# Optimization experiments

Hardware: AMD Instinct MI355X
Metric: run time of the kernel (lower is better)

The kernel has to match this reference:

```python
import jax, jax.numpy as jnp
import numpy as np

N_NODES = 256
DIM = 128
N_LAYERS = 3
LN_EPS = 1e-5


def setup_inputs() -> dict:
    key = jax.random.key(0)
    ks = jax.random.split(key, 8)
    B = 2048
    node_features = jax.random.normal(ks[0], (B, N_NODES, DIM), dtype=jnp.float32)
    A_logits_pos = jax.random.normal(ks[1], (N_NODES, N_NODES), dtype=jnp.float32) * 0.01
    A_logits_neg = jax.random.normal(ks[2], (N_NODES, N_NODES), dtype=jnp.float32) * 0.01
    # per-layer Linear weights, torch layout (out_dim, in_dim); all dims are 128
    scale = 1.0 / np.sqrt(DIM)
    W_pos = jax.random.uniform(ks[3], (N_LAYERS, DIM, DIM), jnp.float32, -scale, scale)
    W_neg = jax.random.uniform(ks[4], (N_LAYERS, DIM, DIM), jnp.float32, -scale, scale)
    ln_g = jnp.ones((N_LAYERS, DIM), jnp.float32)
    ln_b = jnp.zeros((N_LAYERS, DIM), jnp.float32)
    ro_g = jnp.ones((DIM,), jnp.float32)
    ro_b = jnp.zeros((DIM,), jnp.float32)
    return {"node_features": node_features, "A_logits_pos": A_logits_pos,
            "A_logits_neg": A_logits_neg, "W_pos": W_pos, "W_neg": W_neg,
            "ln_g": ln_g, "ln_b": ln_b, "ro_g": ro_g, "ro_b": ro_b}


def _layernorm(x, g, b):
    mu = jnp.mean(x, axis=-1, keepdims=True)
    var = jnp.var(x, axis=-1, keepdims=True)
    return (x - mu) * jax.lax.rsqrt(var + LN_EPS) * g + b


def reference(node_features, A_logits_pos, A_logits_neg, W_pos, W_neg, ln_g, ln_b, ro_g, ro_b):
    # soft signed adjacency with hard-mask split (mask is non-differentiable)
    A_p = jax.nn.sigmoid(A_logits_pos)
    A_n = jax.nn.sigmoid(A_logits_neg)
    mask = (A_p > A_n).astype(A_p.dtype)
    A_pos = A_p * mask
    A_neg = A_n * (1.0 - mask)

    H = node_features  # (B, N, D)
    for l in range(N_LAYERS):
        agg_pos = jnp.einsum('uv,bvd->bud', A_pos, H)
        agg_neg = jnp.einsum('uv,bvd->bud', A_neg, H)
        # torch Linear: x @ W.T ; GELU is exact (erf) by default in torch
        out = jax.nn.gelu(jnp.einsum('bud,od->buo', agg_pos, W_pos[l])
                          - jnp.einsum('bud,od->buo', agg_neg, W_neg[l]),
                          approximate=False)
        H = _layernorm(out, ln_g[l], ln_b[l])  # dropout = identity in eval

    h_G = jnp.mean(H, axis=1)  # (B, D) readout
    return _layernorm(h_G, ro_g, ro_b)
```

## Files before the change

kernel.cpp:

```cpp
#include <hip/hip_runtime.h>
#include <math.h>


typedef float  f32x4  __attribute__((ext_vector_type(4)));
typedef float  f32x16 __attribute__((ext_vector_type(16)));
typedef short  s16x8  __attribute__((ext_vector_type(8)));
typedef __bf16 bf16x8 __attribute__((ext_vector_type(8)));

#define GOFF 65536

__device__ __forceinline__ unsigned short f2bf(float f) {
  __bf16 h = (__bf16)f;
  return __builtin_bit_cast(unsigned short, h);
}
__device__ __forceinline__ float bf2f(unsigned short h) {
  return __builtin_bit_cast(float, (unsigned int)h << 16);
}
__device__ __forceinline__ unsigned short f2bf_rne(float f) {
  unsigned int u = __builtin_bit_cast(unsigned int, f);
  u = (u + 0x7fffu + ((u >> 16) & 1u)) >> 16;
  return (unsigned short)u;
}

__device__ __forceinline__ int haddr(int v, int d) {
  return v * 256 + ((d * 2) ^ ((v & 15) << 4));
}
__device__ __forceinline__ int gaddr(int o, int vr) {
  return GOFF + o * 80 + vr * 2;
}

#define MFMA32(a, b, c) __builtin_amdgcn_mfma_f32_32x32x16_bf16( \
    __builtin_bit_cast(bf16x8, (a)), __builtin_bit_cast(bf16x8, (b)), (c), 0, 0, 0)

__global__ void prep_kernel(const float* __restrict__ alp, const float* __restrict__ aln,
                            const float* __restrict__ wp,  const float* __restrict__ wn,
                            unsigned short* __restrict__ A3, unsigned short* __restrict__ W3) {
  int idx = blockIdx.x * 512 + threadIdx.x;
  if (idx < 131072) {
    int j = idx & 7, lane = (idx >> 3) & 63, vt = (idx >> 9) & 15,
        ut = (idx >> 13) & 7, h = (idx >> 16) & 1;
    int u = ut * 32 + (lane & 31);
    int v = vt * 16 + (lane >> 5) * 8 + j;
    int s = u * 256 + v;
    float ap = 1.f / (1.f + expf(-alp[s]));
    float an = 1.f / (1.f + expf(-aln[s]));
    bool  m  = ap > an;
    float val = h ? (m ? 0.f : -an) : (m ? ap : 0.f);
    A3[idx] = f2bf_rne(val);
  } else {
    int k = idx - 131072;
    int j = k & 7, lane = (k >> 3) & 63, kt = (k >> 9) & 7,
        ot = (k >> 12) & 3, hw = (k >> 14);
    int o = ot * 32 + (lane & 31);
    int d = kt * 16 + (lane >> 5) * 8 + j;
    const float* src = (hw & 1) ? wn : wp;
    W3[k] = f2bf_rne(src[(hw >> 1) * 16384 + o * 128 + d]);
  }
}

__global__ __launch_bounds__(256, 2) void gnn_kernel(
    const float* __restrict__ X,
    const unsigned short* __restrict__ A3,
    const unsigned short* __restrict__ W3,
    const float* __restrict__ ln_g, const float* __restrict__ ln_b,
    const float* __restrict__ ro_g, const float* __restrict__ ro_b,
    float* __restrict__ out) {
  extern __shared__ char smem[];
  const int tid  = threadIdx.x;
  const int wid  = tid >> 6;
  const int lane = tid & 63;
  const int l31  = lane & 31;
  const int hi   = lane >> 5;
  const int b    = blockIdx.x;

  {
    const float4* Xb = (const float4*)(X + (size_t)b * 256 * 128);
#pragma unroll 8
    for (int i = 0; i < 32; ++i) {
      int idx = tid + i * 256;
      int v = idx >> 5, d = (idx & 31) * 4;
      float4 f = Xb[idx];
      ushort4 p;
      p.x = f2bf(f.x); p.y = f2bf(f.y); p.z = f2bf(f.z); p.w = f2bf(f.w);
      *(ushort4*)(smem + haddr(v, d)) = p;
    }
  }
  __syncthreads();

  f32x16 acc[2][4];
  for (int l = 0; l < 3; ++l) {
#pragma unroll
    for (int mt = 0; mt < 2; ++mt)
#pragma unroll
      for (int nt = 0; nt < 4; ++nt)
#pragma unroll
        for (int r = 0; r < 16; ++r) acc[mt][nt][r] = 0.f;

    for (int h = 0; h < 2; ++h) {
      const unsigned short* Wb = W3 + (size_t)(((l * 2 + h) * 4 + wid) * 8) * 512;
      const unsigned short* Ab = A3 + (size_t)((h * 8 + wid * 2) * 16) * 512;

      for (int c = 0; c < 8; ++c) {
        s16x8 pa[4];
#pragma unroll
        for (int kt = 0; kt < 2; ++kt) {
          pa[kt * 2 + 0] = *(const s16x8*)(Ab + (size_t)(0 * 16 + c * 2 + kt) * 512 + lane * 8);
          pa[kt * 2 + 1] = *(const s16x8*)(Ab + (size_t)(1 * 16 + c * 2 + kt) * 512 + lane * 8);
        }

        f32x16 g0;
#pragma unroll
        for (int r = 0; r < 16; ++r) g0[r] = 0.f;
        const int v0 = c * 32 + l31;
#pragma unroll
        for (int kt = 0; kt < 8; ++kt) {
          s16x8 ha = *(const s16x8*)(smem + haddr(v0, kt * 16 + hi * 8));
          s16x8 wb = *(const s16x8*)(Wb + (size_t)kt * 512 + lane * 8);
          g0 = MFMA32(ha, wb, g0);
        }
        __syncthreads();
        {
          const int og = wid * 32 + l31;
#pragma unroll
          for (int rq = 0; rq < 4; ++rq) {
            int vr = rq * 8 + hi * 4;
            ushort4 p;
            p.x = f2bf(g0[rq*4+0]); p.y = f2bf(g0[rq*4+1]);
            p.z = f2bf(g0[rq*4+2]); p.w = f2bf(g0[rq*4+3]);
            *(ushort4*)(smem + gaddr(og, vr)) = p;
          }
        }
        __syncthreads();

#pragma unroll
        for (int kt = 0; kt < 2; ++kt) {
          s16x8 bf[4];
#pragma unroll
          for (int nt = 0; nt < 4; ++nt)
            bf[nt] = *(const s16x8*)(smem + gaddr(nt * 32 + l31, kt * 16 + hi * 8));
#pragma unroll
          for (int nt = 0; nt < 4; ++nt) {
            acc[0][nt] = MFMA32(pa[kt * 2 + 0], bf[nt], acc[0][nt]);
            acc[1][nt] = MFMA32(pa[kt * 2 + 1], bf[nt], acc[1][nt]);
          }
        }
      }
    }

    {
      float lg[4], lb[4];
#pragma unroll
      for (int nt = 0; nt < 4; ++nt) {
        lg[nt] = ln_g[l * 128 + nt * 32 + l31];
        lb[nt] = ln_b[l * 128 + nt * 32 + l31];
      }
#pragma unroll
      for (int mt = 0; mt < 2; ++mt)
#pragma unroll
        for (int r = 0; r < 16; ++r) {
          float x0 = acc[mt][0][r]; x0 = 0.5f * x0 * (1.f + erff(x0 * 0.70710678f));
          float x1 = acc[mt][1][r]; x1 = 0.5f * x1 * (1.f + erff(x1 * 0.70710678f));
          float x2 = acc[mt][2][r]; x2 = 0.5f * x2 * (1.f + erff(x2 * 0.70710678f));
          float x3 = acc[mt][3][r]; x3 = 0.5f * x3 * (1.f + erff(x3 * 0.70710678f));
          acc[mt][0][r] = x0; acc[mt][1][r] = x1;
          acc[mt][2][r] = x2; acc[mt][3][r] = x3;
          float s1 = x0 + x1 + x2 + x3;
          float s2 = x0 * x0 + x1 * x1 + x2 * x2 + x3 * x3;
#pragma unroll
          for (int m = 1; m < 32; m <<= 1) {
            s1 += __shfl_xor(s1, m);
            s2 += __shfl_xor(s2, m);
          }
          float mu  = s1 * (1.f / 128.f);
          float var = s2 * (1.f / 128.f) - mu * mu;
          float rs  = rsqrtf(var + 1e-5f);
          int u = wid * 64 + mt * 32 + (r & 3) + 8 * ((r >> 2) & 3) + 4 * hi;
#pragma unroll
          for (int nt = 0; nt < 4; ++nt) {
            float y = (acc[mt][nt][r] - mu) * rs * lg[nt] + lb[nt];
            *(unsigned short*)(smem + haddr(u, nt * 32 + l31)) = f2bf(y);
          }
        }
    }
    __syncthreads();
  }

  {
    int d   = tid & 127;
    int grp = tid >> 7;
    float s = 0.f;
    for (int v = grp * 128; v < grp * 128 + 128; ++v)
      s += bf2f(*(const unsigned short*)(smem + haddr(v, d)));
    float* red = (float*)(smem + GOFF);
    red[grp * 128 + d] = s;
    __syncthreads();
    if (tid < 128) {
      red[256 + tid] = (red[tid] + red[128 + tid]) * (1.f / 256.f);
    }
    __syncthreads();
    if (tid < 64) {
      float a  = red[256 + tid];
      float b2 = red[256 + 64 + tid];
      float s1 = a + b2, s2 = a * a + b2 * b2;
#pragma unroll
      for (int m = 1; m < 64; m <<= 1) {
        s1 += __shfl_xor(s1, m);
        s2 += __shfl_xor(s2, m);
      }
      float mu  = s1 * (1.f / 128.f);
      float var = s2 * (1.f / 128.f) - mu * mu;
      float rs  = rsqrtf(var + 1e-5f);
      out[(size_t)b * 128 + tid]      = (a  - mu) * rs * ro_g[tid]      + ro_b[tid];
      out[(size_t)b * 128 + 64 + tid] = (b2 - mu) * rs * ro_g[64 + tid] + ro_b[64 + tid];
    }
  }
}

extern "C" void kernel_launch(void* const* d_in, const int* in_sizes, int n_in,
                              void* d_out, int out_size, void* d_ws, size_t ws_size,
                              hipStream_t stream) {
  const float* X   = (const float*)d_in[0];
  const float* alp = (const float*)d_in[1];
  const float* aln = (const float*)d_in[2];
  const float* wp  = (const float*)d_in[3];
  const float* wn  = (const float*)d_in[4];
  const float* lng = (const float*)d_in[5];
  const float* lnb = (const float*)d_in[6];
  const float* rog = (const float*)d_in[7];
  const float* rob = (const float*)d_in[8];
  float* out = (float*)d_out;

  unsigned short* A3 = (unsigned short*)d_ws;
  unsigned short* W3 = A3 + 131072;

  (void)hipFuncSetAttribute(reinterpret_cast<const void*>(gnn_kernel),
                            hipFuncAttributeMaxDynamicSharedMemorySize, 75776);

  prep_kernel<<<448, 512, 0, stream>>>(alp, aln, wp, wn, A3, W3);
  gnn_kernel<<<2048, 256, 75776, stream>>>(X, A3, W3, lng, lnb, rog, rob, out);
}
```

Measured before the change: 734.0 us.

## Split per-layer aggregation into two row passes with register-held weights

Each layer's output rows are now produced in two passes of 32 rows per wave instead of one 64-row pass. This halves the accumulator footprint. The 8 weight fragments are loaded into registers once per sign half rather than per chunk. Pass-0 LayerNorm results are packed as bf16 pairs in registers until pass 1 has finished reading H, then written back to shared memory. In exchange, the H·W product and its block barriers are recomputed in both passes, raising MFMA count and synchronization per layer.

```diff
diff --git a/kernel.cpp b/kernel.cpp
--- a/kernel.cpp
+++ b/kernel.cpp
@@ -87,100 +87,116 @@
   }
   __syncthreads();
 
-  f32x16 acc[2][4];
   for (int l = 0; l < 3; ++l) {
-#pragma unroll
-    for (int mt = 0; mt < 2; ++mt)
+    float lg[4], lb[4];
+#pragma unroll
+    for (int nt = 0; nt < 4; ++nt) {
+      lg[nt] = ln_g[l * 128 + nt * 32 + l31];
+      lb[nt] = ln_b[l * 128 + nt * 32 + l31];
+    }
+    unsigned int hp[32];
+
+#pragma unroll
+    for (int pass = 0; pass < 2; ++pass) {
+      f32x16 acc[4];
 #pragma unroll
       for (int nt = 0; nt < 4; ++nt)
 #pragma unroll
-        for (int r = 0; r < 16; ++r) acc[mt][nt][r] = 0.f;
-
-    for (int h = 0; h < 2; ++h) {
-      const unsigned short* Wb = W3 + (size_t)(((l * 2 + h) * 4 + wid) * 8) * 512;
-      const unsigned short* Ab = A3 + (size_t)((h * 8 + wid * 2) * 16) * 512;
-
-      for (int c = 0; c < 8; ++c) {
-        s16x8 pa[4];
-#pragma unroll
-        for (int kt = 0; kt < 2; ++kt) {
-          pa[kt * 2 + 0] = *(const s16x8*)(Ab + (size_t)(0 * 16 + c * 2 + kt) * 512 + lane * 8);
-          pa[kt * 2 + 1] = *(const s16x8*)(Ab + (size_t)(1 * 16 + c * 2 + kt) * 512 + lane * 8);
-        }
-
-        f32x16 g0;
-#pragma unroll
-        for (int r = 0; r < 16; ++r) g0[r] = 0.f;
-        const int v0 = c * 32 + l31;
-#pragma unroll
-        for (int kt = 0; kt < 8; ++kt) {
-          s16x8 ha = *(const s16x8*)(smem + haddr(v0, kt * 16 + hi * 8));
-          s16x8 wb = *(const s16x8*)(Wb + (size_t)kt * 512 + lane * 8);
-          g0 = MFMA32(ha, wb, g0);
-        }
-        __syncthreads();
-        {
-          const int og = wid * 32 + l31;
-#pragma unroll
-          for (int rq = 0; rq < 4; ++rq) {
-            int vr = rq * 8 + hi * 4;
-            ushort4 p;
-            p.x = f2bf(g0[rq*4+0]); p.y = f2bf(g0[rq*4+1]);
-            p.z = f2bf(g0[rq*4+2]); p.w = f2bf(g0[rq*4+3]);
-            *(ushort4*)(smem + gaddr(og, vr)) = p;
-          }
-        }
-        __syncthreads();
-
-#pragma unroll
-        for (int kt = 0; kt < 2; ++kt) {
-          s16x8 bf[4];
-#pragma unroll
-          for (int nt = 0; nt < 4; ++nt)
-            bf[nt] = *(const s16x8*)(smem + gaddr(nt * 32 + l31, kt * 16 + hi * 8));
+        for (int r = 0; r < 16; ++r) acc[nt][r] = 0.f;
+
+      for (int h = 0; h < 2; ++h) {
+        const unsigned short* Wb = W3 + (size_t)(((l * 2 + h) * 4 + wid) * 8) * 512;
+        const unsigned short* Ab = A3 + (size_t)((h * 8 + pass * 4 + wid) * 16) * 512;
+
+        s16x8 wreg[8];
+#pragma unroll
+        for (int kt = 0; kt < 8; ++kt)
+          wreg[kt] = *(const s16x8*)(Wb + (size_t)kt * 512 + lane * 8);
+
+        for (int c = 0; c < 8; ++c) {
+          f32x16 g0;
+#pragma unroll
+          for (int r = 0; r < 16; ++r) g0[r] = 0.f;
+          const int v0 = c * 32 + l31;
+#pragma unroll
+          for (int kt = 0; kt < 8; ++kt) {
+            s16x8 ha = *(const s16x8*)(smem + haddr(v0, kt * 16 + hi * 8));
+            g0 = MFMA32(ha, wreg[kt], g0);
+          }
+          __syncthreads();
+          {
+            const int og = wid * 32 + l31;
+#pragma unroll
+            for (int rq = 0; rq < 4; ++rq) {
+              int vr = rq * 8 + hi * 4;
+              ushort4 p;
+              p.x = f2bf(g0[rq*4+0]); p.y = f2bf(g0[rq*4+1]);
+              p.z = f2bf(g0[rq*4+2]); p.w = f2bf(g0[rq*4+3]);
+              *(ushort4*)(smem + gaddr(og, vr)) = p;
+            }
+          }
+          __syncthreads();
+
+#pragma unroll
+          for (int kt = 0; kt < 2; ++kt) {
+            s16x8 bf[4];
+#pragma unroll
+            for (int nt = 0; nt < 4; ++nt)
+              bf[nt] = *(const s16x8*)(smem + gaddr(nt * 32 + l31, kt * 16 + hi * 8));
+            s16x8 a0 = *(const s16x8*)(Ab + (size_t)(c * 2 + kt) * 512 + lane * 8);
+#pragma unroll
+            for (int nt = 0; nt < 4; ++nt)
+              acc[nt] = MFMA32(a0, bf[nt], acc[nt]);
+          }
+        }
+      }
+
+#pragma unroll
+      for (int r = 0; r < 16; ++r) {
+        float y[4];
+#pragma unroll
+        for (int nt = 0; nt < 4; ++nt) {
+          float x = acc[nt][r];
+          y[nt] = 0.5f * x * (1.f + erff(x * 0.70710678f));
+        }
+        float s1 = y[0] + y[1] + y[2] + y[3];
+        float s2 = y[0]*y[0] + y[1]*y[1] + y[2]*y[2] + y[3]*y[3];
+#pragma unroll
+        for (int m = 1; m < 32; m <<= 1) {
+          s1 += __shfl_xor(s1, m);
+          s2 += __shfl_xor(s2, m);
+        }
+        float mu  = s1 * (1.f / 128.f);
+        float var = s2 * (1.f / 128.f) - mu * mu;
+        float rs  = rsqrtf(var + 1e-5f);
+        if (pass == 0) {
 #pragma unroll
           for (int nt = 0; nt < 4; ++nt) {
-            acc[0][nt] = MFMA32(pa[kt * 2 + 0], bf[nt], acc[0][nt]);
-            acc[1][nt] = MFMA32(pa[kt * 2 + 1], bf[nt], acc[1][nt]);
-          }
-        }
-      }
-    }
-
-    {
-      float lg[4], lb[4];
+            unsigned int bits = f2bf((y[nt] - mu) * rs * lg[nt] + lb[nt]);
+            if ((r & 1) == 0) hp[nt * 8 + (r >> 1)] = bits;
+            else              hp[nt * 8 + (r >> 1)] |= bits << 16;
+          }
+        } else {
+          int u = 128 + wid * 32 + (r & 3) + 8 * ((r >> 2) & 3) + 4 * hi;
+#pragma unroll
+          for (int nt = 0; nt < 4; ++nt) {
+            float yv = (y[nt] - mu) * rs * lg[nt] + lb[nt];
+            *(unsigned short*)(smem + haddr(u, nt * 32 + l31)) = f2bf(yv);
+          }
+        }
+      }
+    }
+
+#pragma unroll
+    for (int r = 0; r < 16; ++r) {
+      int u = wid * 32 + (r & 3) + 8 * ((r >> 2) & 3) + 4 * hi;
 #pragma unroll
       for (int nt = 0; nt < 4; ++nt) {
-        lg[nt] = ln_g[l * 128 + nt * 32 + l31];
-        lb[nt] = ln_b[l * 128 + nt * 32 + l31];
-      }
-#pragma unroll
-      for (int mt = 0; mt < 2; ++mt)
-#pragma unroll
-        for (int r = 0; r < 16; ++r) {
-          float x0 = acc[mt][0][r]; x0 = 0.5f * x0 * (1.f + erff(x0 * 0.70710678f));
-          float x1 = acc[mt][1][r]; x1 = 0.5f * x1 * (1.f + erff(x1 * 0.70710678f));
-          float x2 = acc[mt][2][r]; x2 = 0.5f * x2 * (1.f + erff(x2 * 0.70710678f));
-          float x3 = acc[mt][3][r]; x3 = 0.5f * x3 * (1.f + erff(x3 * 0.70710678f));
-          acc[mt][0][r] = x0; acc[mt][1][r] = x1;
-          acc[mt][2][r] = x2; acc[mt][3][r] = x3;
-          float s1 = x0 + x1 + x2 + x3;
-          float s2 = x0 * x0 + x1 * x1 + x2 * x2 + x3 * x3;
-#pragma unroll
-          for (int m = 1; m < 32; m <<= 1) {
-            s1 += __shfl_xor(s1, m);
-            s2 += __shfl_xor(s2, m);
-          }
-          float mu  = s1 * (1.f / 128.f);
-          float var = s2 * (1.f / 128.f) - mu * mu;
-          float rs  = rsqrtf(var + 1e-5f);
-          int u = wid * 64 + mt * 32 + (r & 3) + 8 * ((r >> 2) & 3) + 4 * hi;
-#pragma unroll
-          for (int nt = 0; nt < 4; ++nt) {
-            float y = (acc[mt][nt][r] - mu) * rs * lg[nt] + lb[nt];
-            *(unsigned short*)(smem + haddr(u, nt * 32 + l31)) = f2bf(y);
-          }
-        }
+        unsigned int w = hp[nt * 8 + (r >> 1)];
+        unsigned short bits = (r & 1) ? (unsigned short)(w >> 16)
+                                      : (unsigned short)(w & 0xffff);
+        *(unsigned short*)(smem + haddr(u, nt * 32 + l31)) = bits;
+      }
     }
     __syncthreads();
   }
```

Result: slower. 1.734 ms (+136.2%).
